# Kernel optimization log

Measured on AMD Instinct MI355X. Metric: run time of the kernel, lower is better.

## Reference

```python
import jax, jax.numpy as jnp
import numpy as np

B, T, J, D = 2048, 120, 24, 6
E = J * D            # embed_dim = 144
L = 4                # n_layer
NH = 8               # n_head
HD = E // NH         # head_dim = 18
H = 144              # d_model = gru hidden (must equal E, see forward concat)
FF = 4 * E           # transformer dim_feedforward
GIN = E + H          # gru input size


def _layernorm(x, w, b):
    m = x.mean(-1, keepdims=True)
    v = ((x - m) ** 2).mean(-1, keepdims=True)
    return (x - m) / jnp.sqrt(v + 1e-5) * w + b


def setup_inputs() -> dict:
    key = jax.random.key(0)
    ks = jax.random.split(key, 32)
    s = 0.02
    n = lambda k, sh: jax.random.normal(k, sh, jnp.float32) * s
    return {
        "seed": jax.random.normal(ks[0], (B, T, J, D), jnp.float32),
        "qkv_w": n(ks[1], (L, 3 * E, E)), "qkv_b": jnp.zeros((L, 3 * E), jnp.float32),
        "out_w": n(ks[2], (L, E, E)), "out_b": jnp.zeros((L, E), jnp.float32),
        "ln1_w": jnp.ones((L, E), jnp.float32), "ln1_b": jnp.zeros((L, E), jnp.float32),
        "ffn1_w": n(ks[3], (L, FF, E)), "ffn1_b": jnp.zeros((L, FF), jnp.float32),
        "ffn2_w": n(ks[4], (L, E, FF)), "ffn2_b": jnp.zeros((L, E), jnp.float32),
        "ln2_w": jnp.ones((L, E), jnp.float32), "ln2_b": jnp.zeros((L, E), jnp.float32),
        "proj_w": n(ks[5], (E, E)), "proj_b": jnp.zeros((E,), jnp.float32),
        "w_ih": n(ks[6], (3 * H, GIN)), "w_hh": n(ks[7], (3 * H, H)),
        "b_ih": jnp.zeros((3 * H,), jnp.float32), "b_hh": jnp.zeros((3 * H,), jnp.float32),
        "spl_w": n(ks[8], (E, H)), "spl_b": jnp.zeros((E,), jnp.float32),
        "future": 24,
    }


def reference(seed, qkv_w, qkv_b, out_w, out_b, ln1_w, ln1_b, ffn1_w, ffn1_b,
              ffn2_w, ffn2_b, ln2_w, ln2_b, proj_w, proj_b,
              w_ih, w_hh, b_ih, b_hh, spl_w, spl_b, future):
    Bv, Tv, Jv, Dv = seed.shape
    x = seed.reshape(Bv, Tv, Jv * Dv)  # [B, T, E]

    # --- TransformerEncoder (post-norm, relu, dropout=eval-mode identity) ---
    def layer_step(x, p):
        (qw, qb, ow, ob, l1w, l1b, f1w, f1b, f2w, f2b, l2w, l2b) = p
        qkv = jnp.einsum('bse,fe->bsf', x, qw) + qb          # [B,S,3E]
        q, k, v = jnp.split(qkv, 3, axis=-1)
        q = q.reshape(Bv, Tv, NH, HD)
        k = k.reshape(Bv, Tv, NH, HD)
        v = v.reshape(Bv, Tv, NH, HD)
        scores = jnp.einsum('bqhd,bkhd->bhqk', q, k) / jnp.sqrt(jnp.float32(HD))
        attn = jax.nn.softmax(scores, axis=-1)
        o = jnp.einsum('bhqk,bkhd->bqhd', attn, v).reshape(Bv, Tv, E)
        o = jnp.einsum('bse,fe->bsf', o, ow) + ob
        x = _layernorm(x + o, l1w, l1b)
        ff = jax.nn.relu(jnp.einsum('bse,fe->bsf', x, f1w) + f1b)
        ff = jnp.einsum('bsf,ef->bse', ff, f2w) + f2b
        x = _layernorm(x + ff, l2w, l2b)
        return x, None

    x, _ = jax.lax.scan(layer_step, x,
                        (qkv_w, qkv_b, out_w, out_b, ln1_w, ln1_b,
                         ffn1_w, ffn1_b, ffn2_w, ffn2_b, ln2_w, ln2_b))
    ctx = x.mean(axis=1) @ proj_w.T + proj_b               # [B, E]

    h0 = jnp.zeros((Bv, H), seed.dtype)
    inp0 = seed[:, -1].reshape(Bv, Jv * Dv)

    def step(carry, _):
        h, inp = carry
        xc = jnp.concatenate([inp, ctx], axis=-1)          # [B, E+H]
        gi = xc @ w_ih.T + b_ih                            # [B, 3H]
        gh = h @ w_hh.T + b_hh
        ir, iz, in_ = jnp.split(gi, 3, axis=-1)
        hr, hz, hn = jnp.split(gh, 3, axis=-1)
        r = jax.nn.sigmoid(ir + hr)
        z = jax.nn.sigmoid(iz + hz)
        n = jnp.tanh(in_ + r * hn)
        h_new = (1.0 - z) * n + z * h
        rot6d = h_new @ spl_w.T + spl_b                    # [B, E]
        return (h_new, rot6d), rot6d

    _, ys = jax.lax.scan(step, (h0, inp0), None, length=future)  # [future,B,E]
    return ys.transpose(1, 0, 2).reshape(Bv, future, Jv, Dv)
```

## Files before the change

kernel.cpp:

```cpp
#include <hip/hip_runtime.h>

#define B_   2048
#define T_   120
#define E_   144
#define L_   4
#define NH_  8
#define HD_  18
#define FF_  576
#define H_   144
#define GIN_ 288
#define TH_  432
#define FUT_ 24
#define BT_  (B_*T_)

typedef unsigned short u16;
typedef unsigned int   u32;

typedef __attribute__((ext_vector_type(8))) short short8v;
typedef __attribute__((ext_vector_type(4))) float f32x4;

__device__ __forceinline__ float bf2f(u16 u) {
    u32 x = ((u32)u) << 16;
    return __uint_as_float(x);
}
__device__ __forceinline__ u16 f2bf(float f) {
    u32 x = __float_as_uint(f);
    u32 r = (x + 0x7fffu + ((x >> 16) & 1u)) >> 16;
    return (u16)r;
}

struct F4 { float x, y, z, w; };

__device__ __forceinline__ F4 load4(const float* p) {
    float4 v = *(const float4*)p;
    return {v.x, v.y, v.z, v.w};
}
__device__ __forceinline__ void store1(float* p, float v) { *p = v; }
__device__ __forceinline__ void store1(u16* p, float v)   { *p = f2bf(v); }

__device__ __forceinline__ void gll16(const void* g, void* l) {
    __builtin_amdgcn_global_load_lds(
        (const __attribute__((address_space(1))) u32*)g,
        (__attribute__((address_space(3))) u32*)l, 16, 0, 0);
}

__device__ __forceinline__ void stage64(const u16* src, u32* lds, int tid) {
    const char* base = (const char*)src;
    char* lbase = (char*)lds;
    const int w = tid >> 6, l = tid & 63;
#pragma unroll
    for (int i = 0; i < 7; ++i) {
        int inst  = w * 7 + i;
        int chunk = inst * 64 + l;
        int row = chunk / 21;
        int col = chunk - row * 21;
        if (col > 17) col = 17;
        gll16(base + row * 288 + col * 16, lbase + inst * 1024);
    }
}

__global__ void wconv_kernel(const float* __restrict__ src, u16* __restrict__ dst,
                             int rows, int K, int KP, int sstr)
{
    int i = blockIdx.x * 256 + threadIdx.x;
    if (i >= rows * KP) return;
    int r = i / KP, k = i - r * KP;
    dst[i] = (k < K) ? f2bf(src[(size_t)r * sstr + k]) : (u16)0;
}

__global__ void cast_bf_kernel(const float* __restrict__ src, u16* __restrict__ dst,
                               int n2)
{
    int i = blockIdx.x * 256 + threadIdx.x;
    if (i >= n2) return;
    float2 t = ((const float2*)src)[i];
    ((u32*)dst)[i] = ((u32)f2bf(t.y) << 16) | (u32)f2bf(t.x);
}

template<typename OT>
__global__ __launch_bounds__(192) void gemm_mfma(
    const u16* __restrict__ A, const u16* __restrict__ Wb,
    const float* __restrict__ bias, OT* __restrict__ C, int M, int N)
{
    constexpr int RS32 = 84;
    __shared__ u32 lds[64 * RS32];

    const int tid = threadIdx.x;
    const int w   = tid >> 6;
    const int l   = tid & 63;
    const int lg  = l >> 4;
    const int li  = l & 15;
    const int bm  = blockIdx.y * 64;
    const int n0w = blockIdx.x * 144 + w * 48;

    f32x4 acc[4][3];
#pragma unroll
    for (int rt = 0; rt < 4; rt++)
#pragma unroll
        for (int ct = 0; ct < 3; ct++) acc[rt][ct] = {0.f, 0.f, 0.f, 0.f};

    stage64(A + (size_t)bm * 144, lds, tid);
    __syncthreads();

    const u16* lds16 = (const u16*)lds;
#pragma unroll
    for (int s = 0; s < 5; ++s) {
        short8v bf[3];
#pragma unroll
        for (int ct = 0; ct < 3; ++ct) {
            int n = n0w + ct * 16 + li;
            bf[ct] = *(const short8v*)(Wb + (size_t)n * 160 + s * 32 + lg * 8);
        }
        short8v af[4];
#pragma unroll
        for (int rt = 0; rt < 4; ++rt)
            af[rt] = *(const short8v*)(lds16 + (rt * 16 + li) * (2 * RS32) + s * 32 + lg * 8);
#pragma unroll
        for (int rt = 0; rt < 4; ++rt)
#pragma unroll
            for (int ct = 0; ct < 3; ++ct)
                acc[rt][ct] = __builtin_amdgcn_mfma_f32_16x16x32_bf16(
                    af[rt], bf[ct], acc[rt][ct], 0, 0, 0);
    }

#pragma unroll
    for (int ct = 0; ct < 3; ++ct) {
        int col = n0w + ct * 16 + li;
        float bv = bias[col];
#pragma unroll
        for (int rt = 0; rt < 4; ++rt) {
#pragma unroll
            for (int j = 0; j < 4; ++j) {
                int row = bm + rt * 16 + lg * 4 + j;
                store1(&C[(size_t)row * N + col], acc[rt][ct][j] + bv);
            }
        }
    }
}

__global__ __launch_bounds__(192) void olnffn_kernel(
    const u16* __restrict__ ob, const u16* __restrict__ Wo,
    const float* __restrict__ ob_b, const float* __restrict__ res,
    const float* __restrict__ ln1w, const float* __restrict__ ln1b,
    const u16* __restrict__ W1, const float* __restrict__ b1,
    const u16* __restrict__ W2, const float* __restrict__ b2,
    const float* __restrict__ ln2w, const float* __restrict__ ln2b,
    u16* __restrict__ obf, float* __restrict__ of)
{
    constexpr int RSA = 84;
    constexpr int RSF = 52;
    __shared__ u32 Als[64 * RSA];
    __shared__ u32 Fls[64 * RSF];
    __shared__ float lnS[3][64], lnQ[3][64];

    const int tid = threadIdx.x;
    const int w   = tid >> 6;
    const int l   = tid & 63;
    const int lg  = l >> 4;
    const int li  = l & 15;
    const int bm  = blockIdx.x * 64;

    stage64(ob + (size_t)bm * 144, Als, tid);
    __syncthreads();

    const u16* als16 = (const u16*)Als;
    u16* als16w = (u16*)Als;
    u16* fls16 = (u16*)Fls;

    f32x4 acc[4][3];
#pragma unroll
    for (int rt = 0; rt < 4; rt++)
#pragma unroll
        for (int ct = 0; ct < 3; ct++) acc[rt][ct] = {0.f, 0.f, 0.f, 0.f};
#pragma unroll
    for (int s = 0; s < 5; ++s) {
        short8v bf[3];
#pragma unroll
        for (int ct = 0; ct < 3; ++ct) {
            int n = w * 48 + ct * 16 + li;
            bf[ct] = *(const short8v*)(Wo + (size_t)n * 160 + s * 32 + lg * 8);
        }
        short8v af[4];
#pragma unroll
        for (int rt = 0; rt < 4; ++rt)
            af[rt] = *(const short8v*)(als16 + (rt * 16 + li) * (2 * RSA) + s * 32 + lg * 8);
#pragma unroll
        for (int rt = 0; rt < 4; ++rt)
#pragma unroll
            for (int ct = 0; ct < 3; ++ct)
                acc[rt][ct] = __builtin_amdgcn_mfma_f32_16x16x32_bf16(
                    af[rt], bf[ct], acc[rt][ct], 0, 0, 0);
    }

    float vv[4][3][4];
#pragma unroll
    for (int ct = 0; ct < 3; ++ct) {
        int col = w * 48 + ct * 16 + li;
        float bv = ob_b[col];
#pragma unroll
        for (int rt = 0; rt < 4; ++rt)
#pragma unroll
            for (int j = 0; j < 4; ++j) {
                int row = bm + rt * 16 + lg * 4 + j;
                vv[rt][ct][j] = acc[rt][ct][j] + bv + res[(size_t)row * E_ + col];
            }
    }
#pragma unroll
    for (int rt = 0; rt < 4; ++rt)
#pragma unroll
        for (int j = 0; j < 4; ++j) {
            float s = vv[rt][0][j] + vv[rt][1][j] + vv[rt][2][j];
            float q = vv[rt][0][j] * vv[rt][0][j] + vv[rt][1][j] * vv[rt][1][j]
                    + vv[rt][2][j] * vv[rt][2][j];
#pragma unroll
            for (int off = 1; off < 16; off <<= 1) {
                s += __shfl_xor(s, off);
                q += __shfl_xor(q, off);
            }
            if (li == 0) {
                lnS[w][rt * 16 + lg * 4 + j] = s;
                lnQ[w][rt * 16 + lg * 4 + j] = q;
            }
        }
    __syncthreads();
#pragma unroll
    for (int rt = 0; rt < 4; ++rt)
#pragma unroll
        for (int j = 0; j < 4; ++j) {
            int r = rt * 16 + lg * 4 + j;
            float mean = (lnS[0][r] + lnS[1][r] + lnS[2][r]) * (1.f / 144.f);
            float var  = (lnQ[0][r] + lnQ[1][r] + lnQ[2][r]) * (1.f / 144.f) - mean * mean;
            float rstd = rsqrtf(var + 1e-5f);
#pragma unroll
            for (int ct = 0; ct < 3; ++ct) {
                int col = w * 48 + ct * 16 + li;
                float o = (vv[rt][ct][j] - mean) * rstd * ln1w[col] + ln1b[col];
                vv[rt][ct][j] = o;
                als16w[r * (2 * RSA) + col] = f2bf(o);
            }
        }
    __syncthreads();

    f32x4 acc2[4][3];
#pragma unroll
    for (int rt = 0; rt < 4; rt++)
#pragma unroll
        for (int ct = 0; ct < 3; ct++) acc2[rt][ct] = {0.f, 0.f, 0.f, 0.f};

    for (int c = 0; c < 6; ++c) {
        f32x4 acc1[4][2];
#pragma unroll
        for (int rt = 0; rt < 4; rt++)
#pragma unroll
            for (int ct = 0; ct < 2; ct++) acc1[rt][ct] = {0.f, 0.f, 0.f, 0.f};
#pragma unroll
        for (int s = 0; s < 5; ++s) {
            short8v bf[2];
#pragma unroll
            for (int ct = 0; ct < 2; ++ct) {
                int n1 = c * 96 + w * 32 + ct * 16 + li;
                bf[ct] = *(const short8v*)(W1 + (size_t)n1 * 160 + s * 32 + lg * 8);
            }
            short8v af[4];
#pragma unroll
            for (int rt = 0; rt < 4; ++rt)
                af[rt] = *(const short8v*)(als16 + (rt * 16 + li) * (2 * RSA) + s * 32 + lg * 8);
#pragma unroll
            for (int rt = 0; rt < 4; ++rt)
#pragma unroll
                for (int ct = 0; ct < 2; ++ct)
                    acc1[rt][ct] = __builtin_amdgcn_mfma_f32_16x16x32_bf16(
                        af[rt], bf[ct], acc1[rt][ct], 0, 0, 0);
        }
        __syncthreads();
#pragma unroll
        for (int ct = 0; ct < 2; ++ct) {
            int colc = w * 32 + ct * 16 + li;
            float bv = b1[c * 96 + colc];
#pragma unroll
            for (int rt = 0; rt < 4; ++rt)
#pragma unroll
                for (int j = 0; j < 4; ++j) {
                    int row = rt * 16 + lg * 4 + j;
                    float v = fmaxf(acc1[rt][ct][j] + bv, 0.f);
                    fls16[row * (2 * RSF) + colc] = f2bf(v);
                }
        }
        __syncthreads();
#pragma unroll
        for (int s2 = 0; s2 < 3; ++s2) {
            short8v wf[3];
#pragma unroll
            for (int ct = 0; ct < 3; ++ct) {
                int n2 = w * 48 + ct * 16 + li;
                wf[ct] = *(const short8v*)(W2 + (size_t)n2 * 576 + c * 96 + s2 * 32 + lg * 8);
            }
            short8v pf[4];
#pragma unroll
            for (int rt = 0; rt < 4; ++rt)
                pf[rt] = *(const short8v*)(fls16 + (rt * 16 + li) * (2 * RSF) + s2 * 32 + lg * 8);
#pragma unroll
            for (int rt = 0; rt < 4; ++rt)
#pragma unroll
                for (int ct = 0; ct < 3; ++ct)
                    acc2[rt][ct] = __builtin_amdgcn_mfma_f32_16x16x32_bf16(
                        pf[rt], wf[ct], acc2[rt][ct], 0, 0, 0);
        }
    }

    float v2[4][3][4];
#pragma unroll
    for (int ct = 0; ct < 3; ++ct) {
        int col = w * 48 + ct * 16 + li;
        float bv = b2[col];
#pragma unroll
        for (int rt = 0; rt < 4; ++rt)
#pragma unroll
            for (int j = 0; j < 4; ++j)
                v2[rt][ct][j] = acc2[rt][ct][j] + bv + vv[rt][ct][j];
    }
#pragma unroll
    for (int rt = 0; rt < 4; ++rt)
#pragma unroll
        for (int j = 0; j < 4; ++j) {
            float s = v2[rt][0][j] + v2[rt][1][j] + v2[rt][2][j];
            float q = v2[rt][0][j] * v2[rt][0][j] + v2[rt][1][j] * v2[rt][1][j]
                    + v2[rt][2][j] * v2[rt][2][j];
#pragma unroll
            for (int off = 1; off < 16; off <<= 1) {
                s += __shfl_xor(s, off);
                q += __shfl_xor(q, off);
            }
            if (li == 0) {
                lnS[w][rt * 16 + lg * 4 + j] = s;
                lnQ[w][rt * 16 + lg * 4 + j] = q;
            }
        }
    __syncthreads();
#pragma unroll
    for (int rt = 0; rt < 4; ++rt)
#pragma unroll
        for (int j = 0; j < 4; ++j) {
            int r = rt * 16 + lg * 4 + j;
            float mean = (lnS[0][r] + lnS[1][r] + lnS[2][r]) * (1.f / 144.f);
            float var  = (lnQ[0][r] + lnQ[1][r] + lnQ[2][r]) * (1.f / 144.f) - mean * mean;
            float rstd = rsqrtf(var + 1e-5f);
            int row = bm + r;
#pragma unroll
            for (int ct = 0; ct < 3; ++ct) {
                int col = w * 48 + ct * 16 + li;
                float o = (v2[rt][ct][j] - mean) * rstd * ln2w[col] + ln2b[col];
                obf[(size_t)row * E_ + col] = f2bf(o);
                of[(size_t)row * E_ + col]  = o;
            }
        }
}

template<typename AT, typename OT, bool BIAS, bool RELU, bool RES>
__global__ __launch_bounds__(256) void gemm_kernel(
    const AT* __restrict__ A, const float* __restrict__ W, int ldw,
    const float* __restrict__ bias, const float* __restrict__ res,
    OT* __restrict__ C, int M, int N, int K)
{
    constexpr int BM = 64, BN = 64, BK = 16;
    __shared__ float As[BK][BM + 4];
    __shared__ float Ws[BK][BN + 4];
    const int tid = threadIdx.x;
    const int bm = blockIdx.y * BM;
    const int bn = blockIdx.x * BN;
    const int tx = tid & 15, ty = tid >> 4;
    const int lr = tid >> 2;
    const int lc = (tid & 3) << 2;

    float acc[4][4];
#pragma unroll
    for (int i = 0; i < 4; i++)
#pragma unroll
        for (int j = 0; j < 4; j++) acc[i][j] = 0.f;

    for (int k0 = 0; k0 < K; k0 += BK) {
        F4 av = load4(A + (size_t)(bm + lr) * K + k0 + lc);
        As[lc + 0][lr] = av.x; As[lc + 1][lr] = av.y;
        As[lc + 2][lr] = av.z; As[lc + 3][lr] = av.w;
        int n = bn + lr;
        F4 wv = {0.f, 0.f, 0.f, 0.f};
        if (n < N) {
            float4 t = *(const float4*)(W + (size_t)n * ldw + k0 + lc);
            wv = {t.x, t.y, t.z, t.w};
        }
        Ws[lc + 0][lr] = wv.x; Ws[lc + 1][lr] = wv.y;
        Ws[lc + 2][lr] = wv.z; Ws[lc + 3][lr] = wv.w;
        __syncthreads();
#pragma unroll
        for (int kk = 0; kk < BK; ++kk) {
            float a[4], wr[4];
#pragma unroll
            for (int i = 0; i < 4; i++) a[i] = As[kk][ty * 4 + i];
#pragma unroll
            for (int j = 0; j < 4; j++) wr[j] = Ws[kk][tx * 4 + j];
#pragma unroll
            for (int i = 0; i < 4; i++)
#pragma unroll
                for (int j = 0; j < 4; j++) acc[i][j] += a[i] * wr[j];
        }
        __syncthreads();
    }
#pragma unroll
    for (int i = 0; i < 4; i++) {
        int m = bm + ty * 4 + i;
#pragma unroll
        for (int j = 0; j < 4; j++) {
            int n = bn + tx * 4 + j;
            if (n < N) {
                float v = acc[i][j];
                if (BIAS) v += bias[n];
                if (RES)  v += res[(size_t)m * N + n];
                if (RELU) v = fmaxf(v, 0.f);
                store1(&C[(size_t)m * N + n], v);
            }
        }
    }
}

__global__ __launch_bounds__(256) void attn_kernel(const u16* __restrict__ qkv,
                                                   u16* __restrict__ o)
{
    constexpr int QS = 40;
    constexpr int VS = 136;
    __shared__ __align__(16) u16 Qs[128 * QS];
    __shared__ __align__(16) u16 Ks[128 * QS];
    __shared__ __align__(16) u16 Vt[32 * VS];
    __shared__ __align__(16) u16 Ps[4][16 * VS];

    const int bh = blockIdx.x;
    const int b = bh >> 3, h = bh & 7;
    const int tid = threadIdx.x;
    const int w = tid >> 6, l = tid & 63;
    const int lg = l >> 4, li = l & 15;

    {
        u32* z1 = (u32*)Qs;
        for (int i = tid; i < 128 * QS / 2; i += 256) z1[i] = 0;
        u32* z2 = (u32*)Ks;
        for (int i = tid; i < 128 * QS / 2; i += 256) z2[i] = 0;
        u32* z3 = (u32*)Vt;
        for (int i = tid; i < 32 * VS / 2; i += 256) z3[i] = 0;
    }
    __syncthreads();

    const u32* q32 = (const u32*)(qkv + (size_t)b * T_ * TH_);
    for (int idx = tid; idx < 120 * 9; idx += 256) {
        int t = idx / 9, dp = idx - t * 9;
        u32 qv = q32[t * 216 + 9 * h + dp];
        u32 kv = q32[t * 216 + 72 + 9 * h + dp];
        u32 vv = q32[t * 216 + 144 + 9 * h + dp];
        ((u32*)(Qs + t * QS))[dp] = qv;
        ((u32*)(Ks + t * QS))[dp] = kv;
        Vt[(2 * dp) * VS + t]     = (u16)(vv & 0xffffu);
        Vt[(2 * dp + 1) * VS + t] = (u16)(vv >> 16);
    }
    __syncthreads();

    const float scale = 0.23570226039551584f;
    u16* pw = &Ps[w][0];

    for (int mt = w * 2; mt < w * 2 + 2; ++mt) {
        short8v qf = *(const short8v*)(Qs + (mt * 16 + li) * QS + lg * 8);
        f32x4 sacc[8];
#pragma unroll
        for (int nt = 0; nt < 8; ++nt) sacc[nt] = {0.f, 0.f, 0.f, 0.f};
#pragma unroll
        for (int nt = 0; nt < 8; ++nt) {
            short8v kf = *(const short8v*)(Ks + (nt * 16 + li) * QS + lg * 8);
            sacc[nt] = __builtin_amdgcn_mfma_f32_16x16x32_bf16(qf, kf, sacc[nt], 0, 0, 0);
        }

        float invl[4];
#pragma unroll
        for (int j = 0; j < 4; ++j) {
            float v[8];
            float m = -1e30f;
#pragma unroll
            for (int nt = 0; nt < 8; ++nt) {
                float s = sacc[nt][j] * scale;
                if (nt == 7 && li >= 8) s = -1e30f;
                v[nt] = s;
                m = fmaxf(m, s);
            }
#pragma unroll
            for (int off = 1; off < 16; off <<= 1)
                m = fmaxf(m, __shfl_xor(m, off));
            float sum = 0.f;
#pragma unroll
            for (int nt = 0; nt < 8; ++nt) {
                float p = __expf(v[nt] - m);
                sum += p;
                pw[(lg * 4 + j) * VS + nt * 16 + li] = f2bf(p);
            }
#pragma unroll
            for (int off = 1; off < 16; off <<= 1)
                sum += __shfl_xor(sum, off);
            invl[j] = 1.f / sum;
        }

        f32x4 oacc[2] = {{0.f,0.f,0.f,0.f},{0.f,0.f,0.f,0.f}};
#pragma unroll
        for (int s = 0; s < 4; ++s) {
            short8v pf = *(const short8v*)(pw + li * VS + s * 32 + lg * 8);
#pragma unroll
            for (int dt = 0; dt < 2; ++dt) {
                short8v vf = *(const short8v*)(Vt + (dt * 16 + li) * VS + s * 32 + lg * 8);
                oacc[dt] = __builtin_amdgcn_mfma_f32_16x16x32_bf16(pf, vf, oacc[dt], 0, 0, 0);
            }
        }

        const int q0 = mt * 16 + lg * 4;
#pragma unroll
        for (int dt = 0; dt < 2; ++dt) {
            int d = dt * 16 + li;
            if (d < HD_) {
#pragma unroll
                for (int j = 0; j < 4; ++j) {
                    int q = q0 + j;
                    if (q < T_)
                        o[((size_t)b * T_ + q) * E_ + h * HD_ + d] =
                            f2bf(oacc[dt][j] * invl[j]);
                }
            }
        }
    }
}

__global__ void mean_kernel(const float* __restrict__ x, float* __restrict__ out,
                            int nb)
{
    int idx = blockIdx.x * blockDim.x + threadIdx.x;
    if (idx >= nb * E_) return;
    int b = idx / E_, e = idx % E_;
    const float* p = x + (size_t)b * T_ * E_ + e;
    float s = 0.f;
    for (int t = 0; t < T_; t++) s += p[(size_t)t * E_];
    out[idx] = s * (1.f / 120.f);
}

__device__ __forceinline__ float sigmoidf_(float x) {
    return 1.f / (1.f + __expf(-x));
}

#define GRU_M 16
__global__ __launch_bounds__(192) void gru_all_kernel(
    const float* __restrict__ seed,
    const float* __restrict__ gctx,
    const u16* __restrict__ WxB,
    const u16* __restrict__ WhB,
    const u16* __restrict__ SpB,
    const float* __restrict__ b_hh,
    const float* __restrict__ spl_b,
    float* __restrict__ out)
{
    __shared__ __align__(16) u16 xls[GRU_M * 168];
    __shared__ __align__(16) u16 hls[GRU_M * 168];

    const int tid = threadIdx.x;
    const int w = tid >> 6, l = tid & 63;
    const int lg = l >> 4, li = l & 15;
    const int b0 = blockIdx.x * GRU_M;
    const int fr = w * 48 + li;

    for (int i = tid; i < GRU_M * 84; i += 192) {
        ((u32*)xls)[i] = 0; ((u32*)hls)[i] = 0;
    }
    __syncthreads();
    for (int i = tid; i < GRU_M * 72; i += 192) {
        int r = i / 72, e2 = i - r * 72;
        float2 t = *(const float2*)(seed + (size_t)(b0 + r) * T_ * E_
                                    + (size_t)(T_ - 1) * E_ + 2 * e2);
        ((u32*)(xls + r * 168))[e2] = ((u32)f2bf(t.y) << 16) | (u32)f2bf(t.x);
    }

    float gctxv[3][3][4];
    float bhh[3][3];
    float splb[3];
#pragma unroll
    for (int g = 0; g < 3; ++g)
#pragma unroll
        for (int ct = 0; ct < 3; ++ct) {
            int f = g * 144 + fr + ct * 16;
            bhh[g][ct] = b_hh[f];
#pragma unroll
            for (int j = 0; j < 4; ++j)
                gctxv[g][ct][j] = gctx[(size_t)(b0 + lg * 4 + j) * TH_ + f];
        }
#pragma unroll
    for (int ct = 0; ct < 3; ++ct) splb[ct] = spl_b[fr + ct * 16];

    float hold[3][4];
#pragma unroll
    for (int ct = 0; ct < 3; ++ct)
#pragma unroll
        for (int j = 0; j < 4; ++j) hold[ct][j] = 0.f;

    __syncthreads();

    for (int st = 0; st < FUT_; ++st) {
        f32x4 aRZ[2][3], aNi[3], aNh[3];
#pragma unroll
        for (int g = 0; g < 2; ++g)
#pragma unroll
            for (int ct = 0; ct < 3; ++ct) aRZ[g][ct] = {0.f, 0.f, 0.f, 0.f};
#pragma unroll
        for (int ct = 0; ct < 3; ++ct) {
            aNi[ct] = {0.f, 0.f, 0.f, 0.f};
            aNh[ct] = {0.f, 0.f, 0.f, 0.f};
        }
#pragma unroll
        for (int s = 0; s < 5; ++s) {
            short8v ax = *(const short8v*)(xls + li * 168 + s * 32 + lg * 8);
            short8v ah = *(const short8v*)(hls + li * 168 + s * 32 + lg * 8);
#pragma unroll
            for (int ct = 0; ct < 3; ++ct) {
#pragma unroll
                for (int g = 0; g < 2; ++g) {
                    int f = g * 144 + fr + ct * 16;
                    short8v bx = *(const short8v*)(WxB + (size_t)f * 160 + s * 32 + lg * 8);
                    aRZ[g][ct] = __builtin_amdgcn_mfma_f32_16x16x32_bf16(ax, bx, aRZ[g][ct], 0, 0, 0);
                    short8v bh = *(const short8v*)(WhB + (size_t)f * 160 + s * 32 + lg * 8);
                    aRZ[g][ct] = __builtin_amdgcn_mfma_f32_16x16x32_bf16(ah, bh, aRZ[g][ct], 0, 0, 0);
                }
                int f2 = 288 + fr + ct * 16;
                short8v bx2 = *(const short8v*)(WxB + (size_t)f2 * 160 + s * 32 + lg * 8);
                aNi[ct] = __builtin_amdgcn_mfma_f32_16x16x32_bf16(ax, bx2, aNi[ct], 0, 0, 0);
                short8v bh2 = *(const short8v*)(WhB + (size_t)f2 * 160 + s * 32 + lg * 8);
                aNh[ct] = __builtin_amdgcn_mfma_f32_16x16x32_bf16(ah, bh2, aNh[ct], 0, 0, 0);
            }
        }
        __syncthreads();
#pragma unroll
        for (int ct = 0; ct < 3; ++ct)
#pragma unroll
            for (int j = 0; j < 4; ++j) {
                float r = sigmoidf_(aRZ[0][ct][j] + gctxv[0][ct][j] + bhh[0][ct]);
                float z = sigmoidf_(aRZ[1][ct][j] + gctxv[1][ct][j] + bhh[1][ct]);
                float n = tanhf(aNi[ct][j] + gctxv[2][ct][j]
                                + r * (aNh[ct][j] + bhh[2][ct]));
                float hv = (1.f - z) * n + z * hold[ct][j];
                hold[ct][j] = hv;
                hls[(lg * 4 + j) * 168 + fr + ct * 16] = f2bf(hv);
            }
        __syncthreads();
        f32x4 aS[3];
#pragma unroll
        for (int ct = 0; ct < 3; ++ct) aS[ct] = {0.f, 0.f, 0.f, 0.f};
#pragma unroll
        for (int s = 0; s < 5; ++s) {
            short8v ah = *(const short8v*)(hls + li * 168 + s * 32 + lg * 8);
#pragma unroll
            for (int ct = 0; ct < 3; ++ct) {
                short8v bs = *(const short8v*)(SpB + (size_t)(fr + ct * 16) * 160 + s * 32 + lg * 8);
                aS[ct] = __builtin_amdgcn_mfma_f32_16x16x32_bf16(ah, bs, aS[ct], 0, 0, 0);
            }
        }
#pragma unroll
        for (int ct = 0; ct < 3; ++ct) {
            int col = fr + ct * 16;
#pragma unroll
            for (int j = 0; j < 4; ++j) {
                float rv = aS[ct][j] + splb[ct];
                out[(size_t)(b0 + lg * 4 + j) * (FUT_ * E_) + (size_t)st * E_ + col] = rv;
                xls[(lg * 4 + j) * 168 + col] = f2bf(rv);
            }
        }
        __syncthreads();
    }
}

extern "C" void kernel_launch(void* const* d_in, const int* in_sizes, int n_in,
                              void* d_out, int out_size, void* d_ws, size_t ws_size,
                              hipStream_t stream)
{
    const float* seed   = (const float*)d_in[0];
    const float* qkv_w  = (const float*)d_in[1];
    const float* qkv_b  = (const float*)d_in[2];
    const float* out_w  = (const float*)d_in[3];
    const float* out_b  = (const float*)d_in[4];
    const float* ln1_w  = (const float*)d_in[5];
    const float* ln1_b  = (const float*)d_in[6];
    const float* ffn1_w = (const float*)d_in[7];
    const float* ffn1_b = (const float*)d_in[8];
    const float* ffn2_w = (const float*)d_in[9];
    const float* ffn2_b = (const float*)d_in[10];
    const float* ln2_w  = (const float*)d_in[11];
    const float* ln2_b  = (const float*)d_in[12];
    const float* proj_w = (const float*)d_in[13];
    const float* proj_b = (const float*)d_in[14];
    const float* w_ih   = (const float*)d_in[15];
    const float* w_hh   = (const float*)d_in[16];
    const float* b_ih   = (const float*)d_in[17];
    const float* b_hh   = (const float*)d_in[18];
    const float* spl_w  = (const float*)d_in[19];
    const float* spl_b  = (const float*)d_in[20];

    const size_t qkvW_n  = (size_t)L_ * TH_ * 160;
    const size_t outW_n  = (size_t)L_ * E_ * 160;
    const size_t ffn1W_n = (size_t)L_ * FF_ * 160;
    const size_t ffn2W_n = (size_t)L_ * E_ * 576;
    const size_t wxW_n   = (size_t)TH_ * 160;
    const size_t whW_n   = (size_t)TH_ * 160;
    const size_t spW_n   = (size_t)E_ * 160;
    const size_t wbytes  = (qkvW_n + outW_n + ffn1W_n + ffn2W_n
                            + wxW_n + whW_n + spW_n) * 2;

    const size_t persist = (size_t)B_ * 4 * (E_ + E_ + TH_) + wbytes;

    int nc = 16;
    for (int c = 1; c <= 16; c <<= 1) {
        size_t rows = (size_t)(B_ / c) * T_;
        size_t need = persist + rows * 2016;
        if (need <= ws_size) { nc = c; break; }
    }
    const int BC = B_ / nc;
    const int CR = BC * T_;

    char* wsp = (char*)d_ws;
    u16*   xbf   = (u16*)wsp;   wsp += (size_t)CR * E_ * 2;
    float* xres  = (float*)wsp; wsp += (size_t)CR * E_ * 4;
    u16*   qf    = (u16*)wsp;   wsp += (size_t)CR * TH_ * 2;
    u16*   ob    = (u16*)wsp;   wsp += (size_t)CR * E_ * 2;
    float* ctxm  = (float*)wsp; wsp += (size_t)B_ * E_ * 4;
    float* ctx   = (float*)wsp; wsp += (size_t)B_ * E_ * 4;
    float* gctx  = (float*)wsp; wsp += (size_t)B_ * TH_ * 4;
    u16* qkvWb   = (u16*)wsp;   wsp += qkvW_n * 2;
    u16* outWb   = (u16*)wsp;   wsp += outW_n * 2;
    u16* ffn1Wb  = (u16*)wsp;   wsp += ffn1W_n * 2;
    u16* ffn2Wb  = (u16*)wsp;   wsp += ffn2W_n * 2;
    u16* wxB     = (u16*)wsp;   wsp += wxW_n * 2;
    u16* whB     = (u16*)wsp;   wsp += whW_n * 2;
    u16* splWb   = (u16*)wsp;   wsp += spW_n * 2;

    wconv_kernel<<<(int)((qkvW_n + 255) / 256), 256, 0, stream>>>(qkv_w, qkvWb, L_ * TH_, 144, 160, 144);
    wconv_kernel<<<(int)((outW_n + 255) / 256), 256, 0, stream>>>(out_w, outWb, L_ * E_, 144, 160, 144);
    wconv_kernel<<<(int)((ffn1W_n + 255) / 256), 256, 0, stream>>>(ffn1_w, ffn1Wb, L_ * FF_, 144, 160, 144);
    wconv_kernel<<<(int)((ffn2W_n + 255) / 256), 256, 0, stream>>>(ffn2_w, ffn2Wb, L_ * E_, 576, 576, 576);
    wconv_kernel<<<(int)((wxW_n + 255) / 256), 256, 0, stream>>>(w_ih, wxB, TH_, 144, 160, GIN_);
    wconv_kernel<<<(int)((whW_n + 255) / 256), 256, 0, stream>>>(w_hh, whB, TH_, 144, 160, 144);
    wconv_kernel<<<(int)((spW_n + 255) / 256), 256, 0, stream>>>(spl_w, splWb, E_, 144, 160, 144);

    auto grid = [](int M, int N) { return dim3((N + 63) / 64, M / 64); };

    for (int c = 0; c < nc; c++) {
        const int b0 = c * BC;
        cast_bf_kernel<<<(CR * 72 + 255) / 256, 256, 0, stream>>>(
            seed + (size_t)b0 * T_ * E_, xbf, CR * 72);
        const float* resIn = seed + (size_t)b0 * T_ * E_;
        for (int l = 0; l < L_; l++) {
            gemm_mfma<u16><<<dim3(3, CR / 64), 192, 0, stream>>>(
                xbf, qkvWb + (size_t)l * TH_ * 160, qkv_b + (size_t)l * TH_,
                qf, CR, TH_);
            attn_kernel<<<BC * NH_, 256, 0, stream>>>(qf, ob);
            olnffn_kernel<<<CR / 64, 192, 0, stream>>>(
                ob, outWb + (size_t)l * E_ * 160, out_b + (size_t)l * E_, resIn,
                ln1_w + (size_t)l * E_, ln1_b + (size_t)l * E_,
                ffn1Wb + (size_t)l * FF_ * 160, ffn1_b + (size_t)l * FF_,
                ffn2Wb + (size_t)l * E_ * 576, ffn2_b + (size_t)l * E_,
                ln2_w + (size_t)l * E_, ln2_b + (size_t)l * E_, xbf, xres);
            resIn = xres;
        }
        mean_kernel<<<(BC * E_ + 255) / 256, 256, 0, stream>>>(xres, ctxm + (size_t)b0 * E_, BC);
    }

    gemm_kernel<float, float, true, false, false><<<grid(B_, E_), 256, 0, stream>>>(
        ctxm, proj_w, E_, proj_b, nullptr, ctx, B_, E_, E_);
    gemm_kernel<float, float, true, false, false><<<grid(B_, TH_), 256, 0, stream>>>(
        ctx, w_ih + E_, GIN_, b_ih, nullptr, gctx, B_, TH_, E_);

    gru_all_kernel<<<B_ / GRU_M, 192, 0, stream>>>(
        seed, gctx, wxB, whB, splWb, b_hh, spl_b, (float*)d_out);
}
```

Before: 2.778 ms.

## Split olnffn rows across four waves so each wave owns full rows

Result: slower. 3.892 ms (+40.1%).

```diff
diff --git a/kernel.cpp b/kernel.cpp
--- a/kernel.cpp
+++ b/kernel.cpp
@@ -59,6 +59,23 @@
     }
 }
 
+__device__ __forceinline__ void stage64_w4(const u16* src, u32* lds, int tid) {
+    const char* base = (const char*)src;
+    char* lbase = (char*)lds;
+    const int w = tid >> 6, l = tid & 63;
+#pragma unroll
+    for (int i = 0; i < 6; ++i) {
+        int inst = w * 6 + i;
+        if (inst < 21) {
+            int chunk = inst * 64 + l;
+            int row = chunk / 21;
+            int col = chunk - row * 21;
+            if (col > 17) col = 17;
+            gll16(base + row * 288 + col * 16, lbase + inst * 1024);
+        }
+    }
+}
+
 __global__ void wconv_kernel(const float* __restrict__ src, u16* __restrict__ dst,
                              int rows, int K, int KP, int sstr)
 {
@@ -138,7 +155,7 @@
     }
 }
 
-__global__ __launch_bounds__(192) void olnffn_kernel(
+__global__ __launch_bounds__(256) void olnffn_kernel(
     const u16* __restrict__ ob, const u16* __restrict__ Wo,
     const float* __restrict__ ob_b, const float* __restrict__ res,
     const float* __restrict__ ln1w, const float* __restrict__ ln1b,
@@ -147,213 +164,138 @@
     const float* __restrict__ ln2w, const float* __restrict__ ln2b,
     u16* __restrict__ obf, float* __restrict__ of)
 {
-    constexpr int RSA = 84;
-    constexpr int RSF = 52;
-    __shared__ u32 Als[64 * RSA];
-    __shared__ u32 Fls[64 * RSF];
-    __shared__ float lnS[3][64], lnQ[3][64];
+    __shared__ __align__(16) u16 Als[64 * 168];
+    __shared__ __align__(16) u16 Pls[4][16 * 104];
 
     const int tid = threadIdx.x;
-    const int w   = tid >> 6;
-    const int l   = tid & 63;
-    const int lg  = l >> 4;
-    const int li  = l & 15;
-    const int bm  = blockIdx.x * 64;
-
-    stage64(ob + (size_t)bm * 144, Als, tid);
+    const int w  = tid >> 6;
+    const int l  = tid & 63;
+    const int lg = l >> 4;
+    const int li = l & 15;
+    const int bm = blockIdx.x * 64;
+    const int r0 = w * 16;
+
+    stage64_w4(ob + (size_t)bm * 144, (u32*)Als, tid);
     __syncthreads();
 
-    const u16* als16 = (const u16*)Als;
-    u16* als16w = (u16*)Als;
-    u16* fls16 = (u16*)Fls;
-
-    f32x4 acc[4][3];
-#pragma unroll
-    for (int rt = 0; rt < 4; rt++)
-#pragma unroll
-        for (int ct = 0; ct < 3; ct++) acc[rt][ct] = {0.f, 0.f, 0.f, 0.f};
+    const u16* als = Als;
+    u16* alsw = Als;
+    u16* pls = &Pls[w][0];
+
+    f32x4 acc[9];
+#pragma unroll
+    for (int ct = 0; ct < 9; ++ct) acc[ct] = {0.f, 0.f, 0.f, 0.f};
 #pragma unroll
     for (int s = 0; s < 5; ++s) {
-        short8v bf[3];
-#pragma unroll
-        for (int ct = 0; ct < 3; ++ct) {
-            int n = w * 48 + ct * 16 + li;
-            bf[ct] = *(const short8v*)(Wo + (size_t)n * 160 + s * 32 + lg * 8);
-        }
-        short8v af[4];
-#pragma unroll
-        for (int rt = 0; rt < 4; ++rt)
-            af[rt] = *(const short8v*)(als16 + (rt * 16 + li) * (2 * RSA) + s * 32 + lg * 8);
-#pragma unroll
-        for (int rt = 0; rt < 4; ++rt)
-#pragma unroll
-            for (int ct = 0; ct < 3; ++ct)
-                acc[rt][ct] = __builtin_amdgcn_mfma_f32_16x16x32_bf16(
-                    af[rt], bf[ct], acc[rt][ct], 0, 0, 0);
-    }
-
-    float vv[4][3][4];
-#pragma unroll
-    for (int ct = 0; ct < 3; ++ct) {
-        int col = w * 48 + ct * 16 + li;
+        short8v af = *(const short8v*)(als + (r0 + li) * 168 + s * 32 + lg * 8);
+#pragma unroll
+        for (int ct = 0; ct < 9; ++ct) {
+            short8v bf = *(const short8v*)(Wo + (size_t)(ct * 16 + li) * 160 + s * 32 + lg * 8);
+            acc[ct] = __builtin_amdgcn_mfma_f32_16x16x32_bf16(af, bf, acc[ct], 0, 0, 0);
+        }
+    }
+
+    float vv[9][4];
+#pragma unroll
+    for (int ct = 0; ct < 9; ++ct) {
+        int col = ct * 16 + li;
         float bv = ob_b[col];
 #pragma unroll
-        for (int rt = 0; rt < 4; ++rt)
+        for (int j = 0; j < 4; ++j) {
+            int row = bm + r0 + lg * 4 + j;
+            vv[ct][j] = acc[ct][j] + bv + res[(size_t)row * E_ + col];
+        }
+    }
+#pragma unroll
+    for (int j = 0; j < 4; ++j) {
+        float s = 0.f, q = 0.f;
+#pragma unroll
+        for (int ct = 0; ct < 9; ++ct) { s += vv[ct][j]; q += vv[ct][j] * vv[ct][j]; }
+#pragma unroll
+        for (int off = 1; off < 16; off <<= 1) {
+            s += __shfl_xor(s, off);
+            q += __shfl_xor(q, off);
+        }
+        float mean = s * (1.f / 144.f);
+        float var  = q * (1.f / 144.f) - mean * mean;
+        float rstd = rsqrtf(var + 1e-5f);
+        int r = r0 + lg * 4 + j;
+#pragma unroll
+        for (int ct = 0; ct < 9; ++ct) {
+            int col = ct * 16 + li;
+            float o = (vv[ct][j] - mean) * rstd * ln1w[col] + ln1b[col];
+            vv[ct][j] = o;
+            alsw[r * 168 + col] = f2bf(o);
+        }
+    }
+
+    f32x4 acc2[9];
+#pragma unroll
+    for (int ct = 0; ct < 9; ++ct) acc2[ct] = {0.f, 0.f, 0.f, 0.f};
+
+    for (int c = 0; c < 6; ++c) {
+        f32x4 acc1[6];
+#pragma unroll
+        for (int ct = 0; ct < 6; ++ct) acc1[ct] = {0.f, 0.f, 0.f, 0.f};
+#pragma unroll
+        for (int s = 0; s < 5; ++s) {
+            short8v af = *(const short8v*)(als + (r0 + li) * 168 + s * 32 + lg * 8);
+#pragma unroll
+            for (int ct = 0; ct < 6; ++ct) {
+                short8v bf = *(const short8v*)(W1 + (size_t)(c * 96 + ct * 16 + li) * 160 + s * 32 + lg * 8);
+                acc1[ct] = __builtin_amdgcn_mfma_f32_16x16x32_bf16(af, bf, acc1[ct], 0, 0, 0);
+            }
+        }
+#pragma unroll
+        for (int ct = 0; ct < 6; ++ct) {
+            float bv = b1[c * 96 + ct * 16 + li];
 #pragma unroll
             for (int j = 0; j < 4; ++j) {
-                int row = bm + rt * 16 + lg * 4 + j;
-                vv[rt][ct][j] = acc[rt][ct][j] + bv + res[(size_t)row * E_ + col];
-            }
-    }
-#pragma unroll
-    for (int rt = 0; rt < 4; ++rt)
-#pragma unroll
-        for (int j = 0; j < 4; ++j) {
-            float s = vv[rt][0][j] + vv[rt][1][j] + vv[rt][2][j];
-            float q = vv[rt][0][j] * vv[rt][0][j] + vv[rt][1][j] * vv[rt][1][j]
-                    + vv[rt][2][j] * vv[rt][2][j];
-#pragma unroll
-            for (int off = 1; off < 16; off <<= 1) {
-                s += __shfl_xor(s, off);
-                q += __shfl_xor(q, off);
-            }
-            if (li == 0) {
-                lnS[w][rt * 16 + lg * 4 + j] = s;
-                lnQ[w][rt * 16 + lg * 4 + j] = q;
-            }
-        }
-    __syncthreads();
-#pragma unroll
-    for (int rt = 0; rt < 4; ++rt)
-#pragma unroll
-        for (int j = 0; j < 4; ++j) {
-            int r = rt * 16 + lg * 4 + j;
-            float mean = (lnS[0][r] + lnS[1][r] + lnS[2][r]) * (1.f / 144.f);
-            float var  = (lnQ[0][r] + lnQ[1][r] + lnQ[2][r]) * (1.f / 144.f) - mean * mean;
-            float rstd = rsqrtf(var + 1e-5f);
-#pragma unroll
-            for (int ct = 0; ct < 3; ++ct) {
-                int col = w * 48 + ct * 16 + li;
-                float o = (vv[rt][ct][j] - mean) * rstd * ln1w[col] + ln1b[col];
-                vv[rt][ct][j] = o;
-                als16w[r * (2 * RSA) + col] = f2bf(o);
-            }
-        }
-    __syncthreads();
-
-    f32x4 acc2[4][3];
-#pragma unroll
-    for (int rt = 0; rt < 4; rt++)
-#pragma unroll
-        for (int ct = 0; ct < 3; ct++) acc2[rt][ct] = {0.f, 0.f, 0.f, 0.f};
-
-    for (int c = 0; c < 6; ++c) {
-        f32x4 acc1[4][2];
-#pragma unroll
-        for (int rt = 0; rt < 4; rt++)
-#pragma unroll
-            for (int ct = 0; ct < 2; ct++) acc1[rt][ct] = {0.f, 0.f, 0.f, 0.f};
-#pragma unroll
-        for (int s = 0; s < 5; ++s) {
-            short8v bf[2];
-#pragma unroll
-            for (int ct = 0; ct < 2; ++ct) {
-                int n1 = c * 96 + w * 32 + ct * 16 + li;
-                bf[ct] = *(const short8v*)(W1 + (size_t)n1 * 160 + s * 32 + lg * 8);
-            }
-            short8v af[4];
-#pragma unroll
-            for (int rt = 0; rt < 4; ++rt)
-                af[rt] = *(const short8v*)(als16 + (rt * 16 + li) * (2 * RSA) + s * 32 + lg * 8);
-#pragma unroll
-            for (int rt = 0; rt < 4; ++rt)
-#pragma unroll
-                for (int ct = 0; ct < 2; ++ct)
-                    acc1[rt][ct] = __builtin_amdgcn_mfma_f32_16x16x32_bf16(
-                        af[rt], bf[ct], acc1[rt][ct], 0, 0, 0);
-        }
-        __syncthreads();
-#pragma unroll
-        for (int ct = 0; ct < 2; ++ct) {
-            int colc = w * 32 + ct * 16 + li;
-            float bv = b1[c * 96 + colc];
-#pragma unroll
-            for (int rt = 0; rt < 4; ++rt)
-#pragma unroll
-                for (int j = 0; j < 4; ++j) {
-                    int row = rt * 16 + lg * 4 + j;
-                    float v = fmaxf(acc1[rt][ct][j] + bv, 0.f);
-                    fls16[row * (2 * RSF) + colc] = f2bf(v);
-                }
-        }
-        __syncthreads();
+                float v = fmaxf(acc1[ct][j] + bv, 0.f);
+                pls[(lg * 4 + j) * 104 + ct * 16 + li] = f2bf(v);
+            }
+        }
 #pragma unroll
         for (int s2 = 0; s2 < 3; ++s2) {
-            short8v wf[3];
-#pragma unroll
-            for (int ct = 0; ct < 3; ++ct) {
-                int n2 = w * 48 + ct * 16 + li;
-                wf[ct] = *(const short8v*)(W2 + (size_t)n2 * 576 + c * 96 + s2 * 32 + lg * 8);
-            }
-            short8v pf[4];
-#pragma unroll
-            for (int rt = 0; rt < 4; ++rt)
-                pf[rt] = *(const short8v*)(fls16 + (rt * 16 + li) * (2 * RSF) + s2 * 32 + lg * 8);
-#pragma unroll
-            for (int rt = 0; rt < 4; ++rt)
-#pragma unroll
-                for (int ct = 0; ct < 3; ++ct)
-                    acc2[rt][ct] = __builtin_amdgcn_mfma_f32_16x16x32_bf16(
-                        pf[rt], wf[ct], acc2[rt][ct], 0, 0, 0);
-        }
-    }
-
-    float v2[4][3][4];
-#pragma unroll
-    for (int ct = 0; ct < 3; ++ct) {
-        int col = w * 48 + ct * 16 + li;
+            short8v pf = *(const short8v*)(pls + li * 104 + s2 * 32 + lg * 8);
+#pragma unroll
+            for (int ct = 0; ct < 9; ++ct) {
+                short8v wf = *(const short8v*)(W2 + (size_t)(ct * 16 + li) * 576 + c * 96 + s2 * 32 + lg * 8);
+                acc2[ct] = __builtin_amdgcn_mfma_f32_16x16x32_bf16(pf, wf, acc2[ct], 0, 0, 0);
+            }
+        }
+    }
+
+#pragma unroll
+    for (int ct = 0; ct < 9; ++ct) {
+        int col = ct * 16 + li;
         float bv = b2[col];
 #pragma unroll
-        for (int rt = 0; rt < 4; ++rt)
-#pragma unroll
-            for (int j = 0; j < 4; ++j)
-                v2[rt][ct][j] = acc2[rt][ct][j] + bv + vv[rt][ct][j];
-    }
-#pragma unroll
-    for (int rt = 0; rt < 4; ++rt)
-#pragma unroll
-        for (int j = 0; j < 4; ++j) {
-            float s = v2[rt][0][j] + v2[rt][1][j] + v2[rt][2][j];
-            float q = v2[rt][0][j] * v2[rt][0][j] + v2[rt][1][j] * v2[rt][1][j]
-                    + v2[rt][2][j] * v2[rt][2][j];
-#pragma unroll
-            for (int off = 1; off < 16; off <<= 1) {
-                s += __shfl_xor(s, off);
-                q += __shfl_xor(q, off);
-            }
-            if (li == 0) {
-                lnS[w][rt * 16 + lg * 4 + j] = s;
-                lnQ[w][rt * 16 + lg * 4 + j] = q;
-            }
-        }
-    __syncthreads();
-#pragma unroll
-    for (int rt = 0; rt < 4; ++rt)
-#pragma unroll
-        for (int j = 0; j < 4; ++j) {
-            int r = rt * 16 + lg * 4 + j;
-            float mean = (lnS[0][r] + lnS[1][r] + lnS[2][r]) * (1.f / 144.f);
-            float var  = (lnQ[0][r] + lnQ[1][r] + lnQ[2][r]) * (1.f / 144.f) - mean * mean;
-            float rstd = rsqrtf(var + 1e-5f);
-            int row = bm + r;
-#pragma unroll
-            for (int ct = 0; ct < 3; ++ct) {
-                int col = w * 48 + ct * 16 + li;
-                float o = (v2[rt][ct][j] - mean) * rstd * ln2w[col] + ln2b[col];
-                obf[(size_t)row * E_ + col] = f2bf(o);
-                of[(size_t)row * E_ + col]  = o;
-            }
-        }
+        for (int j = 0; j < 4; ++j)
+            vv[ct][j] = acc2[ct][j] + bv + vv[ct][j];
+    }
+#pragma unroll
+    for (int j = 0; j < 4; ++j) {
+        float s = 0.f, q = 0.f;
+#pragma unroll
+        for (int ct = 0; ct < 9; ++ct) { s += vv[ct][j]; q += vv[ct][j] * vv[ct][j]; }
+#pragma unroll
+        for (int off = 1; off < 16; off <<= 1) {
+            s += __shfl_xor(s, off);
+            q += __shfl_xor(q, off);
+        }
+        float mean = s * (1.f / 144.f);
+        float var  = q * (1.f / 144.f) - mean * mean;
+        float rstd = rsqrtf(var + 1e-5f);
+        int row = bm + r0 + lg * 4 + j;
+#pragma unroll
+        for (int ct = 0; ct < 9; ++ct) {
+            int col = ct * 16 + li;
+            float o = (vv[ct][j] - mean) * rstd * ln2w[col] + ln2b[col];
+            obf[(size_t)row * E_ + col] = f2bf(o);
+            of[(size_t)row * E_ + col]  = o;
+        }
+    }
 }
 
 template<typename AT, typename OT, bool BIAS, bool RELU, bool RES>
@@ -757,7 +699,7 @@
                 xbf, qkvWb + (size_t)l * TH_ * 160, qkv_b + (size_t)l * TH_,
                 qf, CR, TH_);
             attn_kernel<<<BC * NH_, 256, 0, stream>>>(qf, ob);
-            olnffn_kernel<<<CR / 64, 192, 0, stream>>>(
+            olnffn_kernel<<<CR / 64, 256, 0, stream>>>(
                 ob, outWb + (size_t)l * E_ * 160, out_b + (size_t)l * E_, resIn,
                 ln1_w + (size_t)l * E_, ln1_b + (size_t)l * E_,
                 ffn1Wb + (size_t)l * FF_ * 160, ffn1_b + (size_t)l * FF_,
```

## Pre-pack weights into MFMA fragment order for coalesced B-operand loads

Applied to the files above, without the earlier changes.

Result: slower. 2.863 ms (+3.0%).

```diff
diff --git a/kernel.cpp b/kernel.cpp
--- a/kernel.cpp
+++ b/kernel.cpp
@@ -38,6 +38,10 @@
 __device__ __forceinline__ void store1(float* p, float v) { *p = v; }
 __device__ __forceinline__ void store1(u16* p, float v)   { *p = f2bf(v); }
 
+__device__ __forceinline__ short8v wfrag(const u16* Wp, int tile, int NS, int s, int l) {
+    return *(const short8v*)(Wp + (((size_t)tile * NS + s) * 64 + l) * 8);
+}
+
 __device__ __forceinline__ void gll16(const void* g, void* l) {
     __builtin_amdgcn_global_load_lds(
         (const __attribute__((address_space(1))) u32*)g,
@@ -59,13 +63,20 @@
     }
 }
 
-__global__ void wconv_kernel(const float* __restrict__ src, u16* __restrict__ dst,
-                             int rows, int K, int KP, int sstr)
+__global__ void wpack_kernel(const float* __restrict__ src, u16* __restrict__ dst,
+                             int ntiles, int NS, int K, int sstr)
 {
     int i = blockIdx.x * 256 + threadIdx.x;
-    if (i >= rows * KP) return;
-    int r = i / KP, k = i - r * KP;
-    dst[i] = (k < K) ? f2bf(src[(size_t)r * sstr + k]) : (u16)0;
+    if (i >= ntiles * NS * 512) return;
+    int e  = i & 7;
+    int l  = (i >> 3) & 63;
+    int c  = i >> 9;
+    int s  = c % NS;
+    int tile = c / NS;
+    int li = l & 15, lg = l >> 4;
+    int row = tile * 16 + li;
+    int k   = s * 32 + lg * 8 + e;
+    dst[i] = (k < K) ? f2bf(src[(size_t)row * sstr + k]) : (u16)0;
 }
 
 __global__ void cast_bf_kernel(const float* __restrict__ src, u16* __restrict__ dst,
@@ -82,8 +93,7 @@
     const u16* __restrict__ A, const u16* __restrict__ Wb,
     const float* __restrict__ bias, OT* __restrict__ C, int M, int N)
 {
-    constexpr int RS32 = 84;
-    __shared__ u32 lds[64 * RS32];
+    __shared__ u32 lds[64 * 84];
 
     const int tid = threadIdx.x;
     const int w   = tid >> 6;
@@ -92,6 +102,7 @@
     const int li  = l & 15;
     const int bm  = blockIdx.y * 64;
     const int n0w = blockIdx.x * 144 + w * 48;
+    const int t0  = blockIdx.x * 9 + w * 3;
 
     f32x4 acc[4][3];
 #pragma unroll
@@ -107,14 +118,12 @@
     for (int s = 0; s < 5; ++s) {
         short8v bf[3];
 #pragma unroll
-        for (int ct = 0; ct < 3; ++ct) {
-            int n = n0w + ct * 16 + li;
-            bf[ct] = *(const short8v*)(Wb + (size_t)n * 160 + s * 32 + lg * 8);
-        }
+        for (int ct = 0; ct < 3; ++ct)
+            bf[ct] = wfrag(Wb, t0 + ct, 5, s, l);
         short8v af[4];
 #pragma unroll
         for (int rt = 0; rt < 4; ++rt)
-            af[rt] = *(const short8v*)(lds16 + (rt * 16 + li) * (2 * RS32) + s * 32 + lg * 8);
+            af[rt] = *(const short8v*)(lds16 + (rt * 16 + li) * 168 + s * 32 + lg * 8);
 #pragma unroll
         for (int rt = 0; rt < 4; ++rt)
 #pragma unroll
@@ -147,10 +156,8 @@
     const float* __restrict__ ln2w, const float* __restrict__ ln2b,
     u16* __restrict__ obf, float* __restrict__ of)
 {
-    constexpr int RSA = 84;
-    constexpr int RSF = 52;
-    __shared__ u32 Als[64 * RSA];
-    __shared__ u32 Fls[64 * RSF];
+    __shared__ __align__(16) u16 Als[64 * 168];
+    __shared__ u32 Fls[64 * 52];
     __shared__ float lnS[3][64], lnQ[3][64];
 
     const int tid = threadIdx.x;
@@ -160,11 +167,11 @@
     const int li  = l & 15;
     const int bm  = blockIdx.x * 64;
 
-    stage64(ob + (size_t)bm * 144, Als, tid);
-    __syncthreads();
-
-    const u16* als16 = (const u16*)Als;
-    u16* als16w = (u16*)Als;
+    stage64(ob + (size_t)bm * 144, (u32*)Als, tid);
+    __syncthreads();
+
+    const u16* als = Als;
+    u16* alsw = Als;
     u16* fls16 = (u16*)Fls;
 
     f32x4 acc[4][3];
@@ -176,14 +183,12 @@
     for (int s = 0; s < 5; ++s) {
         short8v bf[3];
 #pragma unroll
-        for (int ct = 0; ct < 3; ++ct) {
-            int n = w * 48 + ct * 16 + li;
-            bf[ct] = *(const short8v*)(Wo + (size_t)n * 160 + s * 32 + lg * 8);
-        }
+        for (int ct = 0; ct < 3; ++ct)
+            bf[ct] = wfrag(Wo, w * 3 + ct, 5, s, l);
         short8v af[4];
 #pragma unroll
         for (int rt = 0; rt < 4; ++rt)
-            af[rt] = *(const short8v*)(als16 + (rt * 16 + li) * (2 * RSA) + s * 32 + lg * 8);
+            af[rt] = *(const short8v*)(als + (rt * 16 + li) * 168 + s * 32 + lg * 8);
 #pragma unroll
         for (int rt = 0; rt < 4; ++rt)
 #pragma unroll
@@ -236,7 +241,7 @@
                 int col = w * 48 + ct * 16 + li;
                 float o = (vv[rt][ct][j] - mean) * rstd * ln1w[col] + ln1b[col];
                 vv[rt][ct][j] = o;
-                als16w[r * (2 * RSA) + col] = f2bf(o);
+                alsw[r * 168 + col] = f2bf(o);
             }
         }
     __syncthreads();
@@ -257,14 +262,12 @@
         for (int s = 0; s < 5; ++s) {
             short8v bf[2];
 #pragma unroll
-            for (int ct = 0; ct < 2; ++ct) {
-                int n1 = c * 96 + w * 32 + ct * 16 + li;
-                bf[ct] = *(const short8v*)(W1 + (size_t)n1 * 160 + s * 32 + lg * 8);
-            }
+            for (int ct = 0; ct < 2; ++ct)
+                bf[ct] = wfrag(W1, c * 6 + w * 2 + ct, 5, s, l);
             short8v af[4];
 #pragma unroll
             for (int rt = 0; rt < 4; ++rt)
-                af[rt] = *(const short8v*)(als16 + (rt * 16 + li) * (2 * RSA) + s * 32 + lg * 8);
+                af[rt] = *(const short8v*)(als + (rt * 16 + li) * 168 + s * 32 + lg * 8);
 #pragma unroll
             for (int rt = 0; rt < 4; ++rt)
 #pragma unroll
@@ -283,7 +286,7 @@
                 for (int j = 0; j < 4; ++j) {
                     int row = rt * 16 + lg * 4 + j;
                     float v = fmaxf(acc1[rt][ct][j] + bv, 0.f);
-                    fls16[row * (2 * RSF) + colc] = f2bf(v);
+                    fls16[row * 104 + colc] = f2bf(v);
                 }
         }
         __syncthreads();
@@ -291,14 +294,12 @@
         for (int s2 = 0; s2 < 3; ++s2) {
             short8v wf[3];
 #pragma unroll
-            for (int ct = 0; ct < 3; ++ct) {
-                int n2 = w * 48 + ct * 16 + li;
-                wf[ct] = *(const short8v*)(W2 + (size_t)n2 * 576 + c * 96 + s2 * 32 + lg * 8);
-            }
+            for (int ct = 0; ct < 3; ++ct)
+                wf[ct] = wfrag(W2, w * 3 + ct, 18, c * 3 + s2, l);
             short8v pf[4];
 #pragma unroll
             for (int rt = 0; rt < 4; ++rt)
-                pf[rt] = *(const short8v*)(fls16 + (rt * 16 + li) * (2 * RSF) + s2 * 32 + lg * 8);
+                pf[rt] = *(const short8v*)(fls16 + (rt * 16 + li) * 104 + s2 * 32 + lg * 8);
 #pragma unroll
             for (int rt = 0; rt < 4; ++rt)
 #pragma unroll
@@ -621,16 +622,16 @@
             for (int ct = 0; ct < 3; ++ct) {
 #pragma unroll
                 for (int g = 0; g < 2; ++g) {
-                    int f = g * 144 + fr + ct * 16;
-                    short8v bx = *(const short8v*)(WxB + (size_t)f * 160 + s * 32 + lg * 8);
+                    int tile = g * 9 + w * 3 + ct;
+                    short8v bx = wfrag(WxB, tile, 5, s, l);
                     aRZ[g][ct] = __builtin_amdgcn_mfma_f32_16x16x32_bf16(ax, bx, aRZ[g][ct], 0, 0, 0);
-                    short8v bh = *(const short8v*)(WhB + (size_t)f * 160 + s * 32 + lg * 8);
+                    short8v bh = wfrag(WhB, tile, 5, s, l);
                     aRZ[g][ct] = __builtin_amdgcn_mfma_f32_16x16x32_bf16(ah, bh, aRZ[g][ct], 0, 0, 0);
                 }
-                int f2 = 288 + fr + ct * 16;
-                short8v bx2 = *(const short8v*)(WxB + (size_t)f2 * 160 + s * 32 + lg * 8);
+                int tile2 = 18 + w * 3 + ct;
+                short8v bx2 = wfrag(WxB, tile2, 5, s, l);
                 aNi[ct] = __builtin_amdgcn_mfma_f32_16x16x32_bf16(ax, bx2, aNi[ct], 0, 0, 0);
-                short8v bh2 = *(const short8v*)(WhB + (size_t)f2 * 160 + s * 32 + lg * 8);
+                short8v bh2 = wfrag(WhB, tile2, 5, s, l);
                 aNh[ct] = __builtin_amdgcn_mfma_f32_16x16x32_bf16(ah, bh2, aNh[ct], 0, 0, 0);
             }
         }
@@ -656,7 +657,7 @@
             short8v ah = *(const short8v*)(hls + li * 168 + s * 32 + lg * 8);
 #pragma unroll
             for (int ct = 0; ct < 3; ++ct) {
-                short8v bs = *(const short8v*)(SpB + (size_t)(fr + ct * 16) * 160 + s * 32 + lg * 8);
+                short8v bs = wfrag(SpB, w * 3 + ct, 5, s, l);
                 aS[ct] = __builtin_amdgcn_mfma_f32_16x16x32_bf16(ah, bs, aS[ct], 0, 0, 0);
             }
         }
@@ -737,13 +738,13 @@
     u16* whB     = (u16*)wsp;   wsp += whW_n * 2;
     u16* splWb   = (u16*)wsp;   wsp += spW_n * 2;
 
-    wconv_kernel<<<(int)((qkvW_n + 255) / 256), 256, 0, stream>>>(qkv_w, qkvWb, L_ * TH_, 144, 160, 144);
-    wconv_kernel<<<(int)((outW_n + 255) / 256), 256, 0, stream>>>(out_w, outWb, L_ * E_, 144, 160, 144);
-    wconv_kernel<<<(int)((ffn1W_n + 255) / 256), 256, 0, stream>>>(ffn1_w, ffn1Wb, L_ * FF_, 144, 160, 144);
-    wconv_kernel<<<(int)((ffn2W_n + 255) / 256), 256, 0, stream>>>(ffn2_w, ffn2Wb, L_ * E_, 576, 576, 576);
-    wconv_kernel<<<(int)((wxW_n + 255) / 256), 256, 0, stream>>>(w_ih, wxB, TH_, 144, 160, GIN_);
-    wconv_kernel<<<(int)((whW_n + 255) / 256), 256, 0, stream>>>(w_hh, whB, TH_, 144, 160, 144);
-    wconv_kernel<<<(int)((spW_n + 255) / 256), 256, 0, stream>>>(spl_w, splWb, E_, 144, 160, 144);
+    wpack_kernel<<<(int)((qkvW_n + 255) / 256), 256, 0, stream>>>(qkv_w, qkvWb, L_ * 27, 5, 144, 144);
+    wpack_kernel<<<(int)((outW_n + 255) / 256), 256, 0, stream>>>(out_w, outWb, L_ * 9, 5, 144, 144);
+    wpack_kernel<<<(int)((ffn1W_n + 255) / 256), 256, 0, stream>>>(ffn1_w, ffn1Wb, L_ * 36, 5, 144, 144);
+    wpack_kernel<<<(int)((ffn2W_n + 255) / 256), 256, 0, stream>>>(ffn2_w, ffn2Wb, L_ * 9, 18, 576, 576);
+    wpack_kernel<<<(int)((wxW_n + 255) / 256), 256, 0, stream>>>(w_ih, wxB, 27, 5, 144, GIN_);
+    wpack_kernel<<<(int)((whW_n + 255) / 256), 256, 0, stream>>>(w_hh, whB, 27, 5, 144, 144);
+    wpack_kernel<<<(int)((spW_n + 255) / 256), 256, 0, stream>>>(spl_w, splWb, 9, 5, 144, 144);
 
     auto grid = [](int M, int N) { return dim3((N + 63) / 64, M / 64); };
 
```
